# Optimization experiments

Measured on AMD Instinct MI355X. Metric: run time of the kernel, lower is better.

The kernel has to match this reference:

```python
import jax, jax.numpy as jnp
import numpy as np

R, B, D, H, N, F = 8, 16, 32, 128, 2048, 256
HALF_LOG_2PI = np.float32(0.9189385332046727)  # 0.5*log(2*pi)


def _made_masks():
    # MADE masks for a 2-hidden-layer network (D -> H -> H -> 2*D), params=2,
    # input_order='random' per (region, batch) network, hidden degrees cyclic in [1, D-1].
    rng = np.random.RandomState(0)
    deg_in = np.stack([np.stack([rng.permutation(D) + 1 for _ in range(B)]) for _ in range(R)])  # [R,B,D]
    h_deg = (np.arange(H) % (D - 1)) + 1  # [H]
    M1 = (deg_in[:, :, :, None] <= h_deg[None, None, None, :]).astype(np.float32)  # [R,B,D,H]
    M2 = np.broadcast_to((h_deg[:, None] <= h_deg[None, :]).astype(np.float32), (R, B, H, H)).copy()  # [R,B,H,H]
    out_deg = np.repeat(deg_in, 2, axis=-1)  # [R,B,2D]; index k=2*d+p matches reshape(...,D,2)
    M3 = (h_deg[None, None, :, None] < out_deg[:, :, None, :]).astype(np.float32)  # [R,B,H,2D]
    return M1, M2, M3


def setup_inputs() -> dict:
    key = jax.random.key(0)
    k1, k2, k3, k4 = jax.random.split(key, 4)
    x = jax.random.normal(k1, (N, F), dtype=jnp.float32)
    W1 = jax.random.normal(k2, (R, B, D, H), dtype=jnp.float32) * 0.1
    W2 = jax.random.normal(k3, (R, B, H, H), dtype=jnp.float32) * 0.05
    W3 = jax.random.normal(k4, (R, B, H, 2 * D), dtype=jnp.float32) * 0.02
    M1, M2, M3 = _made_masks()
    region_idx = jnp.arange(F, dtype=jnp.int64 if jax.config.jax_enable_x64 else jnp.int32).reshape(R, D)
    return {"x": x, "W1": W1, "W2": W2, "W3": W3,
            "M1": jnp.asarray(M1), "M2": jnp.asarray(M2), "M3": jnp.asarray(M3),
            "region_idx": region_idx}


def reference(x, W1, W2, W3, M1, M2, M3, region_idx):
    # Gather per-region features: [N, R, D] -> [R, N, D]
    xr = jnp.transpose(x[:, region_idx], (1, 0, 2))
    # Masked MADE forward (no bias, relu), batched over all R*B networks.
    h1 = jax.nn.relu(jnp.einsum('rnd,rbdh->rbnh', xr, W1 * M1))
    h2 = jax.nn.relu(jnp.einsum('rbnh,rbhk->rbnk', h1, W2 * M2))
    out = jnp.einsum('rbnk,rbko->rbno', h2, W3 * M3)  # [R,B,N,2D]
    out = out.reshape(out.shape[0], out.shape[1], out.shape[2], -1, 2)  # [R,B,N,D,2]
    shift, log_scale = out[..., 0], out[..., 1]
    # MAF inverse (one pass): u = (y - shift) * exp(-log_scale);
    # log_prob = sum_d Normal(0,1).log_prob(u_d) - log_scale_d
    u = (xr[:, None] - shift) * jnp.exp(-log_scale)  # [R,B,N,D]
    ll = jnp.sum(-0.5 * u * u - HALF_LOG_2PI - log_scale, axis=-1)  # [R,B,N]
    return jnp.transpose(ll, (2, 0, 1))  # [N, R, B]
```

## Files before the change

### kernel.cpp

```cpp
#include <hip/hip_runtime.h>
#include <math.h>

constexpr int R_ = 8;
constexpr int B_ = 16;
constexpr int D_ = 32;
constexpr int H_ = 128;
constexpr int N_ = 2048;
constexpr int F_ = 256;
constexpr int O_ = 64;
constexpr float HLP_ = 0.9189385332046727f;

typedef float f32x4 __attribute__((ext_vector_type(4)));
typedef short bf16x8 __attribute__((ext_vector_type(8)));
typedef unsigned uint32x4 __attribute__((ext_vector_type(4)));

__device__ __forceinline__ unsigned pk2(float lo, float hi) {
    unsigned a = __builtin_bit_cast(unsigned, lo) + 0x8000u;
    unsigned b = __builtin_bit_cast(unsigned, hi) + 0x8000u;
    return __builtin_amdgcn_perm(b, a, 0x07060302);
}

__global__ __launch_bounds__(256, 2)
void flow_all(const float* __restrict__ x,
              const float* __restrict__ W1, const float* __restrict__ W2,
              const float* __restrict__ W3,
              const float* __restrict__ M1, const float* __restrict__ M2,
              const float* __restrict__ M3,
              const int* __restrict__ ridx,
              float* __restrict__ out)
{
    __shared__ __align__(16) unsigned short WA2[16384];
    __shared__ __align__(16) unsigned short uni[16384];

    const int bid = blockIdx.x;
    const int rb  = bid >> 2;
    const int sl  = bid & 3;
    const int r   = rb >> 4;

    const int t    = threadIdx.x;
    const int lane = t & 63;
    const int w    = t >> 6;
    const int q    = lane >> 4;
    const int c    = lane & 15;

    unsigned short* stg0 = uni;
    unsigned short* stg1 = uni + 5120;
    unsigned short* hwp  = uni + w * 4096;

    const int nbase = sl * 512 + w * 128 + c;
    const int xoff  = r * 32 + q * 8;

    auto xload = [&](int row, float* g) {
        const float* p0 = x + (size_t)row * F_ + xoff;
        float4 f0 = *(const float4*)p0;
        float4 f1 = *(const float4*)(p0 + 4);
        g[0] = f0.x; g[1] = f0.y; g[2] = f0.z; g[3] = f0.w;
        g[4] = f1.x; g[5] = f1.y; g[6] = f1.z; g[7] = f1.w;
    };

    bf16x8 a1[8], a3[4][4];
    {
        const float* W1b = W1 + (size_t)rb * 32 * 128;
        const float* M1b = M1 + (size_t)rb * 32 * 128;
        const float* W2b = W2 + (size_t)rb * 128 * 128;
        const float* M2s = M2;
        const float* W3b = W3 + (size_t)rb * 128 * 64;
        const float* M3b = M3 + (size_t)rb * 128 * 64;

        const int pm = t & 127, pkh = t >> 7;
        const int qm = t & 63,  qk  = t >> 6;
        int osrc;
        {
            int dp = qm >> 1, pb = qm & 1;
            int dsrc = ((dp >> 1) & 3) * 8 + (dp >> 3) * 2 + (dp & 1);
            osrc = dsrc * 2 + pb;
        }

        float wv[2][16], mv[2][16];
        auto slab_load = [&](int s, float* wvv, float* mvv) {
            if (s == 0) {
                const float* wp = W1b + (size_t)(pkh * 16) * 128 + pm;
                const float* mp = M1b + (size_t)(pkh * 16) * 128 + pm;
#pragma unroll
                for (int e = 0; e < 16; ++e) { wvv[e] = wp[(size_t)e * 128]; mvv[e] = mp[(size_t)e * 128]; }
            } else if (s <= 4) {
                const float* wp = W2b + (size_t)((s - 1) * 32 + pkh * 16) * 128 + pm;
                const float* mp = M2s + (size_t)((s - 1) * 32 + pkh * 16) * 128 + pm;
#pragma unroll
                for (int e = 0; e < 16; ++e) { wvv[e] = wp[(size_t)e * 128]; mvv[e] = mp[(size_t)e * 128]; }
            } else {
                int ss = s - 5;
                const float* wp = W3b + (size_t)(ss * 64 + qk * 16) * 64 + osrc;
                const float* mp = M3b + (size_t)(ss * 64 + qk * 16) * 64 + osrc;
#pragma unroll
                for (int e = 0; e < 16; ++e) { wvv[e] = wp[(size_t)e * 64]; mvv[e] = mp[(size_t)e * 64]; }
            }
        };
        auto pack8 = [&](const float* wvv, const float* mvv, unsigned* u) {
#pragma unroll
            for (int e2 = 0; e2 < 8; ++e2)
                u[e2] = pk2(wvv[2 * e2] * mvv[2 * e2], wvv[2 * e2 + 1] * mvv[2 * e2 + 1]);
        };
        auto store_stg128 = [&](unsigned short* st, const float* wvv, const float* mvv) {
            unsigned u[8]; pack8(wvv, mvv, u);
            *(uint32x4*)&st[pm * 40 + pkh * 16]     = (uint32x4){u[0], u[1], u[2], u[3]};
            *(uint32x4*)&st[pm * 40 + pkh * 16 + 8] = (uint32x4){u[4], u[5], u[6], u[7]};
        };
        auto store_stg64 = [&](unsigned short* st, const float* wvv, const float* mvv) {
            unsigned u[8]; pack8(wvv, mvv, u);
            *(uint32x4*)&st[qm * 72 + qk * 16]     = (uint32x4){u[0], u[1], u[2], u[3]};
            *(uint32x4*)&st[qm * 72 + qk * 16 + 8] = (uint32x4){u[4], u[5], u[6], u[7]};
        };
        auto store_wa2 = [&](int kt, const float* wvv, const float* mvv) {
            unsigned u[8]; pack8(wvv, mvv, u);
            int mt = pm >> 4, cc = pm & 15, q0 = pkh * 2;
            *(uint32x4*)&WA2[(((kt * 8 + mt) * 64) + q0 * 16 + cc) * 8]       = (uint32x4){u[0], u[1], u[2], u[3]};
            *(uint32x4*)&WA2[(((kt * 8 + mt) * 64) + (q0 + 1) * 16 + cc) * 8] = (uint32x4){u[4], u[5], u[6], u[7]};
        };

        slab_load(0, wv[0], mv[0]);
        slab_load(1, wv[1], mv[1]);
        store_stg128(stg0, wv[0], mv[0]);
        __syncthreads();
#pragma unroll
        for (int mt = 0; mt < 8; ++mt)
            a1[mt] = *(const bf16x8*)&stg0[(mt * 16 + c) * 40 + q * 8];
        slab_load(2, wv[0], mv[0]);
        store_wa2(0, wv[1], mv[1]);
        slab_load(3, wv[1], mv[1]);
        store_wa2(1, wv[0], mv[0]);
        slab_load(4, wv[0], mv[0]);
        store_wa2(2, wv[1], mv[1]);
        slab_load(5, wv[1], mv[1]);
        store_wa2(3, wv[0], mv[0]);
        slab_load(6, wv[0], mv[0]);
        store_stg64(stg1, wv[1], mv[1]);
        __syncthreads();
#pragma unroll
        for (int mt3 = 0; mt3 < 4; ++mt3) {
            a3[0][mt3] = *(const bf16x8*)&stg1[(mt3 * 16 + c) * 72 + 0  + q * 8];
            a3[1][mt3] = *(const bf16x8*)&stg1[(mt3 * 16 + c) * 72 + 32 + q * 8];
        }
        store_stg64(stg0, wv[0], mv[0]);
        __syncthreads();
#pragma unroll
        for (int mt3 = 0; mt3 < 4; ++mt3) {
            a3[2][mt3] = *(const bf16x8*)&stg0[(mt3 * 16 + c) * 72 + 0  + q * 8];
            a3[3][mt3] = *(const bf16x8*)&stg0[(mt3 * 16 + c) * 72 + 32 + q * 8];
        }
    }
    __syncthreads();

    auto hstore = [&](int tau, int mt, const f32x4& v) {
        int ktw = mt >> 1;
        int qw  = (mt & 1) * 2 + (q >> 1);
        int j0  = (q & 1) * 4;
        unsigned lo = pk2(fmaxf(v[0], 0.f), fmaxf(v[1], 0.f));
        unsigned hi = pk2(fmaxf(v[2], 0.f), fmaxf(v[3], 0.f));
        *(uint2*)&hwp[(((tau * 4 + ktw) * 64) + qw * 16 + c) * 8 + j0] = make_uint2(lo, hi);
    };

    const f32x4 z = {0.f, 0.f, 0.f, 0.f};

#pragma unroll 1
    for (int p = 0; p < 4; ++p) {
        float xA[8], xB[8];
        xload(nbase + p * 32,      xA);
        xload(nbase + p * 32 + 16, xB);
        uint32x4 uA = {pk2(xA[0], xA[1]), pk2(xA[2], xA[3]), pk2(xA[4], xA[5]), pk2(xA[6], xA[7])};
        uint32x4 uB = {pk2(xB[0], xB[1]), pk2(xB[2], xB[3]), pk2(xB[4], xB[5]), pk2(xB[6], xB[7])};
        bf16x8 xbA = __builtin_bit_cast(bf16x8, uA);
        bf16x8 xbB = __builtin_bit_cast(bf16x8, uB);

        {
            f32x4 accA[8], accB[8];
#pragma unroll
            for (int mt = 0; mt < 8; ++mt) {
                accA[mt] = __builtin_amdgcn_mfma_f32_16x16x32_bf16(a1[mt], xbA, z, 0, 0, 0);
                accB[mt] = __builtin_amdgcn_mfma_f32_16x16x32_bf16(a1[mt], xbB, z, 0, 0, 0);
            }
#pragma unroll
            for (int mt = 0; mt < 8; ++mt) { hstore(0, mt, accA[mt]); hstore(1, mt, accB[mt]); }
        }

        {
            f32x4 c2A[8], c2B[8];
#pragma unroll
            for (int mt = 0; mt < 8; ++mt) { c2A[mt] = z; c2B[mt] = z; }
#pragma unroll
            for (int kt = 0; kt < 4; ++kt) {
                bf16x8 bA = *(const bf16x8*)&hwp[((0 * 4 + kt) * 64 + lane) * 8];
                bf16x8 bB = *(const bf16x8*)&hwp[((1 * 4 + kt) * 64 + lane) * 8];
                bf16x8 a2t[8];
#pragma unroll
                for (int mt = 0; mt < 8; ++mt)
                    a2t[mt] = *(const bf16x8*)&WA2[((kt * 8 + mt) * 64 + lane) * 8];
#pragma unroll
                for (int mt = 0; mt < 8; ++mt) {
                    c2A[mt] = __builtin_amdgcn_mfma_f32_16x16x32_bf16(a2t[mt], bA, c2A[mt], 0, 0, 0);
                    c2B[mt] = __builtin_amdgcn_mfma_f32_16x16x32_bf16(a2t[mt], bB, c2B[mt], 0, 0, 0);
                }
            }
#pragma unroll
            for (int mt = 0; mt < 8; ++mt) { hstore(0, mt, c2A[mt]); hstore(1, mt, c2B[mt]); }
        }

        {
            f32x4 c3A[4], c3B[4];
#pragma unroll
            for (int mt3 = 0; mt3 < 4; ++mt3) { c3A[mt3] = z; c3B[mt3] = z; }
#pragma unroll
            for (int kt = 0; kt < 4; ++kt) {
                bf16x8 bA = *(const bf16x8*)&hwp[((0 * 4 + kt) * 64 + lane) * 8];
                bf16x8 bB = *(const bf16x8*)&hwp[((1 * 4 + kt) * 64 + lane) * 8];
#pragma unroll
                for (int mt3 = 0; mt3 < 4; ++mt3) {
                    c3A[mt3] = __builtin_amdgcn_mfma_f32_16x16x32_bf16(a3[kt][mt3], bA, c3A[mt3], 0, 0, 0);
                    c3B[mt3] = __builtin_amdgcn_mfma_f32_16x16x32_bf16(a3[kt][mt3], bB, c3B[mt3], 0, 0, 0);
                }
            }
            float llA = 0.f, llB = 0.f;
#pragma unroll
            for (int mt3 = 0; mt3 < 4; ++mt3) {
#pragma unroll
                for (int rr = 0; rr < 2; ++rr) {
                    float shA = c3A[mt3][rr * 2], lsA = c3A[mt3][rr * 2 + 1];
                    float shB = c3B[mt3][rr * 2], lsB = c3B[mt3][rr * 2 + 1];
                    float u0 = (xA[mt3 * 2 + rr] - shA) * __expf(-lsA);
                    float u1 = (xB[mt3 * 2 + rr] - shB) * __expf(-lsB);
                    llA += fmaf(-0.5f * u0, u0, -HLP_ - lsA);
                    llB += fmaf(-0.5f * u1, u1, -HLP_ - lsB);
                }
            }
            llA += __shfl_xor(llA, 16, 64);  llA += __shfl_xor(llA, 32, 64);
            llB += __shfl_xor(llB, 16, 64);  llB += __shfl_xor(llB, 32, 64);
            if (q == 0) {
                int n = nbase + p * 32;
                out[(size_t)n * 128 + rb]        = llA;
                out[(size_t)(n + 16) * 128 + rb] = llB;
            }
        }
    }
}

extern "C" void kernel_launch(void* const* d_in, const int* in_sizes, int n_in,
                              void* d_out, int out_size, void* d_ws, size_t ws_size,
                              hipStream_t stream) {
    const float* x   = (const float*)d_in[0];
    const float* W1  = (const float*)d_in[1];
    const float* W2  = (const float*)d_in[2];
    const float* W3  = (const float*)d_in[3];
    const float* M1  = (const float*)d_in[4];
    const float* M2  = (const float*)d_in[5];
    const float* M3  = (const float*)d_in[6];
    const int*  ridx = (const int*)d_in[7];
    float* out = (float*)d_out;

    flow_all<<<dim3(512), dim3(256), 0, stream>>>(x, W1, W2, W3, M1, M2, M3, ridx, out);
}
```

Before: 108.7 us.

## Use 512-thread blocks covering half of N and prefetch next x tile

Doubles the block size to 8 waves so each block handles 1024 rows of one network, halving the grid to 256 blocks. Each block now stages the masked weights once for twice as many rows, and the per-thread weight staging load is halved. Each wave gets its own h buffer, separate from the staging area. The x rows for the next iteration are prefetched into registers after the first GEMM, overlapping global latency with compute. Risks: higher LDS use per block (about 112KB) may limit occupancy to one block per CU, and a grid of 256 blocks may underfill the 256 CUs.

```diff
diff --git a/kernel.cpp b/kernel.cpp
--- a/kernel.cpp
+++ b/kernel.cpp
@@ -20,7 +20,7 @@
     return __builtin_amdgcn_perm(b, a, 0x07060302);
 }
 
-__global__ __launch_bounds__(256, 2)
+__global__ __launch_bounds__(512, 2)
 void flow_all(const float* __restrict__ x,
               const float* __restrict__ W1, const float* __restrict__ W2,
               const float* __restrict__ W3,
@@ -30,11 +30,12 @@
               float* __restrict__ out)
 {
     __shared__ __align__(16) unsigned short WA2[16384];
-    __shared__ __align__(16) unsigned short uni[16384];
+    __shared__ __align__(16) unsigned short stg[2][5120];
+    __shared__ __align__(16) unsigned short hws[8][4096];
 
     const int bid = blockIdx.x;
-    const int rb  = bid >> 2;
-    const int sl  = bid & 3;
+    const int rb  = bid >> 1;
+    const int hf  = bid & 1;
     const int r   = rb >> 4;
 
     const int t    = threadIdx.x;
@@ -43,11 +44,9 @@
     const int q    = lane >> 4;
     const int c    = lane & 15;
 
-    unsigned short* stg0 = uni;
-    unsigned short* stg1 = uni + 5120;
-    unsigned short* hwp  = uni + w * 4096;
-
-    const int nbase = sl * 512 + w * 128 + c;
+    unsigned short* hwp = hws[w];
+
+    const int nbase = hf * 1024 + w * 128 + c;
     const int xoff  = r * 32 + q * 8;
 
     auto xload = [&](int row, float* g) {
@@ -57,6 +56,10 @@
         g[0] = f0.x; g[1] = f0.y; g[2] = f0.z; g[3] = f0.w;
         g[4] = f1.x; g[5] = f1.y; g[6] = f1.z; g[7] = f1.w;
     };
+
+    float gA[8], gB[8];
+    xload(nbase, gA);
+    xload(nbase + 16, gB);
 
     bf16x8 a1[8], a3[4][4];
     {
@@ -76,55 +79,52 @@
             osrc = dsrc * 2 + pb;
         }
 
-        float wv[2][16], mv[2][16];
+        float wv[2][8], mv[2][8];
         auto slab_load = [&](int s, float* wvv, float* mvv) {
             if (s == 0) {
-                const float* wp = W1b + (size_t)(pkh * 16) * 128 + pm;
-                const float* mp = M1b + (size_t)(pkh * 16) * 128 + pm;
-#pragma unroll
-                for (int e = 0; e < 16; ++e) { wvv[e] = wp[(size_t)e * 128]; mvv[e] = mp[(size_t)e * 128]; }
+                const float* wp = W1b + (size_t)(pkh * 8) * 128 + pm;
+                const float* mp = M1b + (size_t)(pkh * 8) * 128 + pm;
+#pragma unroll
+                for (int e = 0; e < 8; ++e) { wvv[e] = wp[(size_t)e * 128]; mvv[e] = mp[(size_t)e * 128]; }
             } else if (s <= 4) {
-                const float* wp = W2b + (size_t)((s - 1) * 32 + pkh * 16) * 128 + pm;
-                const float* mp = M2s + (size_t)((s - 1) * 32 + pkh * 16) * 128 + pm;
-#pragma unroll
-                for (int e = 0; e < 16; ++e) { wvv[e] = wp[(size_t)e * 128]; mvv[e] = mp[(size_t)e * 128]; }
+                const float* wp = W2b + (size_t)((s - 1) * 32 + pkh * 8) * 128 + pm;
+                const float* mp = M2s + (size_t)((s - 1) * 32 + pkh * 8) * 128 + pm;
+#pragma unroll
+                for (int e = 0; e < 8; ++e) { wvv[e] = wp[(size_t)e * 128]; mvv[e] = mp[(size_t)e * 128]; }
             } else {
                 int ss = s - 5;
-                const float* wp = W3b + (size_t)(ss * 64 + qk * 16) * 64 + osrc;
-                const float* mp = M3b + (size_t)(ss * 64 + qk * 16) * 64 + osrc;
-#pragma unroll
-                for (int e = 0; e < 16; ++e) { wvv[e] = wp[(size_t)e * 64]; mvv[e] = mp[(size_t)e * 64]; }
-            }
-        };
-        auto pack8 = [&](const float* wvv, const float* mvv, unsigned* u) {
-#pragma unroll
-            for (int e2 = 0; e2 < 8; ++e2)
+                const float* wp = W3b + (size_t)(ss * 64 + qk * 8) * 64 + osrc;
+                const float* mp = M3b + (size_t)(ss * 64 + qk * 8) * 64 + osrc;
+#pragma unroll
+                for (int e = 0; e < 8; ++e) { wvv[e] = wp[(size_t)e * 64]; mvv[e] = mp[(size_t)e * 64]; }
+            }
+        };
+        auto pack4 = [&](const float* wvv, const float* mvv, unsigned* u) {
+#pragma unroll
+            for (int e2 = 0; e2 < 4; ++e2)
                 u[e2] = pk2(wvv[2 * e2] * mvv[2 * e2], wvv[2 * e2 + 1] * mvv[2 * e2 + 1]);
         };
         auto store_stg128 = [&](unsigned short* st, const float* wvv, const float* mvv) {
-            unsigned u[8]; pack8(wvv, mvv, u);
-            *(uint32x4*)&st[pm * 40 + pkh * 16]     = (uint32x4){u[0], u[1], u[2], u[3]};
-            *(uint32x4*)&st[pm * 40 + pkh * 16 + 8] = (uint32x4){u[4], u[5], u[6], u[7]};
+            unsigned u[4]; pack4(wvv, mvv, u);
+            *(uint32x4*)&st[pm * 40 + pkh * 8] = (uint32x4){u[0], u[1], u[2], u[3]};
         };
         auto store_stg64 = [&](unsigned short* st, const float* wvv, const float* mvv) {
-            unsigned u[8]; pack8(wvv, mvv, u);
-            *(uint32x4*)&st[qm * 72 + qk * 16]     = (uint32x4){u[0], u[1], u[2], u[3]};
-            *(uint32x4*)&st[qm * 72 + qk * 16 + 8] = (uint32x4){u[4], u[5], u[6], u[7]};
+            unsigned u[4]; pack4(wvv, mvv, u);
+            *(uint32x4*)&st[qm * 72 + qk * 8] = (uint32x4){u[0], u[1], u[2], u[3]};
         };
         auto store_wa2 = [&](int kt, const float* wvv, const float* mvv) {
-            unsigned u[8]; pack8(wvv, mvv, u);
-            int mt = pm >> 4, cc = pm & 15, q0 = pkh * 2;
-            *(uint32x4*)&WA2[(((kt * 8 + mt) * 64) + q0 * 16 + cc) * 8]       = (uint32x4){u[0], u[1], u[2], u[3]};
-            *(uint32x4*)&WA2[(((kt * 8 + mt) * 64) + (q0 + 1) * 16 + cc) * 8] = (uint32x4){u[4], u[5], u[6], u[7]};
+            unsigned u[4]; pack4(wvv, mvv, u);
+            int mt = pm >> 4, cc = pm & 15;
+            *(uint32x4*)&WA2[(((kt * 8 + mt) * 64) + pkh * 16 + cc) * 8] = (uint32x4){u[0], u[1], u[2], u[3]};
         };
 
         slab_load(0, wv[0], mv[0]);
         slab_load(1, wv[1], mv[1]);
-        store_stg128(stg0, wv[0], mv[0]);
+        store_stg128(stg[0], wv[0], mv[0]);
         __syncthreads();
 #pragma unroll
         for (int mt = 0; mt < 8; ++mt)
-            a1[mt] = *(const bf16x8*)&stg0[(mt * 16 + c) * 40 + q * 8];
+            a1[mt] = *(const bf16x8*)&stg[0][(mt * 16 + c) * 40 + q * 8];
         slab_load(2, wv[0], mv[0]);
         store_wa2(0, wv[1], mv[1]);
         slab_load(3, wv[1], mv[1]);
@@ -134,19 +134,19 @@
         slab_load(5, wv[1], mv[1]);
         store_wa2(3, wv[0], mv[0]);
         slab_load(6, wv[0], mv[0]);
-        store_stg64(stg1, wv[1], mv[1]);
+        store_stg64(stg[1], wv[1], mv[1]);
         __syncthreads();
 #pragma unroll
         for (int mt3 = 0; mt3 < 4; ++mt3) {
-            a3[0][mt3] = *(const bf16x8*)&stg1[(mt3 * 16 + c) * 72 + 0  + q * 8];
-            a3[1][mt3] = *(const bf16x8*)&stg1[(mt3 * 16 + c) * 72 + 32 + q * 8];
-        }
-        store_stg64(stg0, wv[0], mv[0]);
+            a3[0][mt3] = *(const bf16x8*)&stg[1][(mt3 * 16 + c) * 72 + 0  + q * 8];
+            a3[1][mt3] = *(const bf16x8*)&stg[1][(mt3 * 16 + c) * 72 + 32 + q * 8];
+        }
+        store_stg64(stg[0], wv[0], mv[0]);
         __syncthreads();
 #pragma unroll
         for (int mt3 = 0; mt3 < 4; ++mt3) {
-            a3[2][mt3] = *(const bf16x8*)&stg0[(mt3 * 16 + c) * 72 + 0  + q * 8];
-            a3[3][mt3] = *(const bf16x8*)&stg0[(mt3 * 16 + c) * 72 + 32 + q * 8];
+            a3[2][mt3] = *(const bf16x8*)&stg[0][(mt3 * 16 + c) * 72 + 0  + q * 8];
+            a3[3][mt3] = *(const bf16x8*)&stg[0][(mt3 * 16 + c) * 72 + 32 + q * 8];
         }
     }
     __syncthreads();
@@ -165,8 +165,8 @@
 #pragma unroll 1
     for (int p = 0; p < 4; ++p) {
         float xA[8], xB[8];
-        xload(nbase + p * 32,      xA);
-        xload(nbase + p * 32 + 16, xB);
+#pragma unroll
+        for (int j = 0; j < 8; ++j) { xA[j] = gA[j]; xB[j] = gB[j]; }
         uint32x4 uA = {pk2(xA[0], xA[1]), pk2(xA[2], xA[3]), pk2(xA[4], xA[5]), pk2(xA[6], xA[7])};
         uint32x4 uB = {pk2(xB[0], xB[1]), pk2(xB[2], xB[3]), pk2(xB[4], xB[5]), pk2(xB[6], xB[7])};
         bf16x8 xbA = __builtin_bit_cast(bf16x8, uA);
@@ -181,6 +181,11 @@
             }
 #pragma unroll
             for (int mt = 0; mt < 8; ++mt) { hstore(0, mt, accA[mt]); hstore(1, mt, accB[mt]); }
+        }
+
+        if (p < 3) {
+            xload(nbase + (p + 1) * 32, gA);
+            xload(nbase + (p + 1) * 32 + 16, gB);
         }
 
         {
@@ -256,5 +261,5 @@
     const int*  ridx = (const int*)d_in[7];
     float* out = (float*)d_out;
 
-    flow_all<<<dim3(512), dim3(256), 0, stream>>>(x, W1, W2, W3, M1, M2, M3, ridx, out);
+    flow_all<<<dim3(256), dim3(512), 0, stream>>>(x, W1, W2, W3, M1, M2, M3, ridx, out);
 }
```

Result: no change. 108.4 us (-0.3%).
